# Kernel tuning notes

Measured on AMD Instinct MI355X. Metric: run time of the kernel, lower is better.

## Reference

```python
import jax, jax.numpy as jnp
import numpy as np

K_HEADS = 8
D_HEAD = 8
C_IN = 128   # c_x + c_t after channel concat
C_OUT = K_HEADS * D_HEAD  # 64
SMALL = -32767.0  # -2**15 + 1


def setup_inputs() -> dict:
    key = jax.random.key(0)
    ks = jax.random.split(key, 12)
    B, Cx, V, T = 8, 64, 200, 128
    x = jax.random.normal(ks[0], (B, Cx, V, T), dtype=jnp.float32)
    tem_embedding = jax.random.normal(ks[1], (B, Cx, V, T), dtype=jnp.float32)
    s = 0.05
    Wq = jax.random.normal(ks[2], (C_OUT, C_IN), dtype=jnp.float32) * s
    bq = jax.random.normal(ks[3], (C_OUT,), dtype=jnp.float32) * s
    Wk = jax.random.normal(ks[4], (C_OUT, C_IN), dtype=jnp.float32) * s
    bk = jax.random.normal(ks[5], (C_OUT,), dtype=jnp.float32) * s
    Wv = jax.random.normal(ks[6], (C_OUT, C_IN), dtype=jnp.float32) * s
    bv = jax.random.normal(ks[7], (C_OUT,), dtype=jnp.float32) * s
    Wo = jax.random.normal(ks[8], (C_OUT, C_OUT), dtype=jnp.float32) * s
    bo = jax.random.normal(ks[9], (C_OUT,), dtype=jnp.float32) * s
    return {"x": x, "tem_embedding": tem_embedding,
            "Wq": Wq, "bq": bq, "Wk": Wk, "bk": bk,
            "Wv": Wv, "bv": bv, "Wo": Wo, "bo": bo}


def reference(x, tem_embedding, Wq, bq, Wk, bk, Wv, bv, Wo, bo):
    B, _, V, T = x.shape
    # concat temporal embedding on channel dim (last T steps)
    xt = jnp.concatenate([x, tem_embedding[:, :, :, -T:]], axis=1)  # [B, C_IN, V, T]

    def proj(W, b):  # 1x1 conv == channel einsum
        return jnp.einsum('oi,bivt->bovt', W, xt) + b[None, :, None, None]

    def heads(t):  # [B, K*d, V, T] -> [K*B, V, T, d] (split on dim1, cat on dim0)
        t = t.reshape(B, K_HEADS, D_HEAD, V, T)
        t = jnp.transpose(t, (1, 0, 3, 4, 2))  # [K, B, V, T, d]
        return t.reshape(K_HEADS * B, V, T, D_HEAD)

    q = heads(proj(Wq, bq))
    k = heads(proj(Wk, bk))
    v = heads(proj(Wv, bv))

    attn = jnp.einsum('nvtd,nvsd->nvts', q, k) / jnp.sqrt(jnp.float32(D_HEAD))
    causal = jnp.tril(jnp.ones((T, T), dtype=bool))  # [T, T]
    attn = jnp.where(causal[None, None, :, :], attn, SMALL)
    attn = jax.nn.softmax(attn, axis=-1)
    out = jnp.einsum('nvts,nvsd->nvtd', attn, v)  # [K*B, V, T, d]

    # merge heads back: [K*B, V, T, d] -> [B, K*d, V, T]
    out = out.reshape(K_HEADS, B, V, T, D_HEAD)
    out = jnp.transpose(out, (1, 0, 4, 2, 3)).reshape(B, K_HEADS * D_HEAD, V, T)
    out = jnp.einsum('oi,bivt->bovt', Wo, out) + bo[None, :, None, None]
    return jax.nn.relu(out)
```

## Files before the change

### kernel.cpp

```cpp
#include <hip/hip_runtime.h>
#include <stdint.h>

#define TPB 512

constexpr int Bb   = 8;
constexpr int Vv   = 200;
constexpr int Tt   = 128;
constexpr int CIN  = 128;
constexpr int COUT = 64;

typedef __attribute__((ext_vector_type(8))) short bf16x8;
typedef __attribute__((ext_vector_type(4))) short short4v;
typedef __attribute__((ext_vector_type(4))) float f32x4;

__device__ __forceinline__ unsigned short f2bf(float f) {
    union { float f; unsigned u; } x; x.f = f;
    unsigned r = x.u + 0x7fffu + ((x.u >> 16) & 1u);
    return (unsigned short)(r >> 16);
}
__device__ __forceinline__ unsigned pk2(float a, float b) {
    return (unsigned)f2bf(a) | ((unsigned)f2bf(b) << 16);
}

#if __has_builtin(__builtin_amdgcn_mfma_f32_16x16x16bf16_1k)
#define MFMA16(a, b, c) __builtin_amdgcn_mfma_f32_16x16x16bf16_1k(a, b, c, 0, 0, 0)
#else
__device__ __forceinline__ f32x4 mfma16_asm(short4v a, short4v b, f32x4 c) {
    f32x4 d;
    asm("v_mfma_f32_16x16x16_bf16 %0, %1, %2, %3" : "=v"(d) : "v"(a), "v"(b), "v"(c));
    return d;
}
#define MFMA16(a, b, c) mfma16_asm(a, b, c)
#endif

__global__ __launch_bounds__(TPB, 6)
void tatt_fused(const float* __restrict__ x, const float* __restrict__ tem,
                const float* __restrict__ Wq, const float* __restrict__ bq,
                const float* __restrict__ Wk, const float* __restrict__ bk,
                const float* __restrict__ Wv, const float* __restrict__ bv,
                const float* __restrict__ Wo, const float* __restrict__ bo,
                float* __restrict__ out)
{
    __shared__ __align__(16) unsigned char smem[53248];
    unsigned short* qk = (unsigned short*)smem;
    unsigned short* vt = (unsigned short*)(smem + 32768);
    unsigned short* ot = (unsigned short*)(smem + 32768);
    unsigned short* xt = (unsigned short*)(smem + 49152);

    const int tid = threadIdx.x;
    const int w = tid >> 6, lane = tid & 63;
    const int l15 = lane & 15, qd = lane >> 4;
    const int b = blockIdx.x / Vv, v = blockIdx.x % Vv;
    const float QS = 1.44269504088896f * 0.35355339059327f;

    bf16x8 afr0[4], afr1[4];
    {
        const float* W0 = (w < 4) ? Wq : Wv;
        const int o0_ = (w < 4) ? w : (w - 4);
        const float* base0 = W0 + (o0_ * 16 + l15) * CIN + qd * 8;
        #pragma unroll
        for (int kc = 0; kc < 4; ++kc) {
            float4 fa = *(const float4*)(base0 + kc * 32);
            float4 fb = *(const float4*)(base0 + kc * 32 + 4);
            union { bf16x8 v8; unsigned u[4]; } t;
            t.u[0] = pk2(fa.x, fa.y); t.u[1] = pk2(fa.z, fa.w);
            t.u[2] = pk2(fb.x, fb.y); t.u[3] = pk2(fb.z, fb.w);
            afr0[kc] = t.v8;
        }
        if (w < 4) {
            const float* base1 = Wk + (w * 16 + l15) * CIN + qd * 8;
            #pragma unroll
            for (int kc = 0; kc < 4; ++kc) {
                float4 fa = *(const float4*)(base1 + kc * 32);
                float4 fb = *(const float4*)(base1 + kc * 32 + 4);
                union { bf16x8 v8; unsigned u[4]; } t;
                t.u[0] = pk2(fa.x, fa.y); t.u[1] = pk2(fa.z, fa.w);
                t.u[2] = pk2(fb.x, fb.y); t.u[3] = pk2(fb.z, fb.w);
                afr1[kc] = t.v8;
            }
        }
    }

    auto tileC = [&](const bf16x8 (&A)[4], int p, int ot_, int r) {
        f32x4 acc = {0.f, 0.f, 0.f, 0.f};
        const unsigned short* Bbp = xt + l15 * CIN;
        #pragma unroll
        for (int kc = 0; kc < 4; ++kc) {
            int phys = (kc * 4 + qd) ^ l15;
            bf16x8 bb = *(const bf16x8*)(Bbp + phys * 8);
            acc = __builtin_amdgcn_mfma_f32_16x16x32_bf16(A[kc], bb, acc, 0, 0, 0);
        }
        const int obase = ot_ * 16 + qd * 4;
        const float* bp = (p == 0) ? bq : ((p == 1) ? bk : bv);
        float4 bias = *(const float4*)(bp + obase);
        float bb4[4] = {bias.x, bias.y, bias.z, bias.w};
        const int tg = r * 16 + l15;
        if (p == 2) {
            #pragma unroll
            for (int rr = 0; rr < 4; ++rr) {
                int dg = obase + rr;
                int tp = tg ^ ((((dg >> 2) & 3)) << 4);
                vt[dg * 128 + tp] = f2bf(acc[rr] + bb4[rr]);
            }
        } else {
            float sc = (p == 0) ? QS : 1.0f;
            ushort4 s4;
            s4.x = f2bf((acc[0] + bb4[0]) * sc);
            s4.y = f2bf((acc[1] + bb4[1]) * sc);
            s4.z = f2bf((acc[2] + bb4[2]) * sc);
            s4.w = f2bf((acc[3] + bb4[3]) * sc);
            int phys = (obase >> 2) ^ (tg & 14);
            *(ushort4*)(qk + p * 8192 + tg * 64 + phys * 4) = s4;
        }
    };

    {
        const int sc_ = tid >> 2;
        const int stq = tid & 3;
        const float* sbase = (sc_ < 64 ? x : tem)
            + ((b * 64 + (sc_ & 63)) * Vv + v) * Tt + stq * 4;
        float4 pf = *(const float4*)(sbase);
        const int clow = sc_ & 7, chi = sc_ >> 3;

        for (int r = 0; r < 8; ++r) {
            if (r) __syncthreads();
            {
                int t0 = stq * 4;
                xt[(t0 + 0) * CIN + ((chi ^ (t0 + 0)) << 3) + clow] = f2bf(pf.x);
                xt[(t0 + 1) * CIN + ((chi ^ (t0 + 1)) << 3) + clow] = f2bf(pf.y);
                xt[(t0 + 2) * CIN + ((chi ^ (t0 + 2)) << 3) + clow] = f2bf(pf.z);
                xt[(t0 + 3) * CIN + ((chi ^ (t0 + 3)) << 3) + clow] = f2bf(pf.w);
            }
            if (r < 7) pf = *(const float4*)(sbase + (r + 1) * 16);
            __syncthreads();
            if (w < 4) { tileC(afr0, 0, w, r); tileC(afr1, 1, w, r); }
            else       { tileC(afr0, 2, w - 4, r); }
        }
    }
    __syncthreads();

    {
        const int h = w;
        const int qkoff = ((h * 2 + qd) ^ (l15 & 14)) << 2;
        short4v vfrag[8];
        short4v qfrag[8];
        {
            const int dg = h * 8 + l15;
            const int swz = ((dg >> 2) & 3) << 4;
            #pragma unroll
            for (int st = 0; st < 8; ++st) {
                short4v f = {0, 0, 0, 0};
                if (l15 < 8) {
                    int sp = (st * 16 + qd * 4) ^ swz;
                    f = *(const short4v*)(vt + dg * 128 + sp);
                }
                vfrag[st] = f;
            }
            #pragma unroll
            for (int st = 0; st < 8; ++st) {
                short4v qf = {0, 0, 0, 0};
                if (qd < 2) qf = *(const short4v*)(qk + (st * 16 + l15) * 64 + qkoff);
                qfrag[st] = qf;
            }
        }
        __syncthreads();

        bool dmask[4];
        #pragma unroll
        for (int r = 0; r < 4; ++r) dmask[r] = (qd * 4 + r) <= l15;

        #pragma unroll
        for (int tt = 0; tt < 8; ++tt) {
            f32x4 o0 = {0.f, 0.f, 0.f, 0.f}, o1 = {0.f, 0.f, 0.f, 0.f};
            float lac = 0.f;
            #pragma unroll
            for (int st = 0; st < 8; ++st) {
                if (st <= tt) {
                    short4v kf = {0, 0, 0, 0};
                    if (qd < 2) kf = *(const short4v*)(qk + 8192 + (st * 16 + l15) * 64 + qkoff);
                    f32x4 z = {0.f, 0.f, 0.f, 0.f};
                    f32x4 s = MFMA16(kf, qfrag[tt], z);
                    float p0 = __builtin_amdgcn_exp2f(s[0]);
                    float p1 = __builtin_amdgcn_exp2f(s[1]);
                    float p2 = __builtin_amdgcn_exp2f(s[2]);
                    float p3 = __builtin_amdgcn_exp2f(s[3]);
                    if (st == tt) {
                        p0 = dmask[0] ? p0 : 0.f;
                        p1 = dmask[1] ? p1 : 0.f;
                        p2 = dmask[2] ? p2 : 0.f;
                        p3 = dmask[3] ? p3 : 0.f;
                    }
                    lac += (p0 + p1) + (p2 + p3);
                    int pp0 = (int)pk2(p0, p1), pp1 = (int)pk2(p2, p3);
                    short4v pf;
                    pf[0] = (short)(pp0 & 0xffff); pf[1] = (short)(pp0 >> 16);
                    pf[2] = (short)(pp1 & 0xffff); pf[3] = (short)(pp1 >> 16);
                    if (st & 1) o1 = MFMA16(vfrag[st], pf, o1);
                    else        o0 = MFMA16(vfrag[st], pf, o0);
                }
            }
            float l = lac;
            l += __shfl_xor(l, 16, 64);
            l += __shfl_xor(l, 32, 64);
            float rl = __builtin_amdgcn_rcpf(l);
            if (qd < 2) {
                float r0 = (o0[0] + o1[0]) * rl, r1 = (o0[1] + o1[1]) * rl;
                float r2 = (o0[2] + o1[2]) * rl, r3 = (o0[3] + o1[3]) * rl;
                int t = tt * 16 + l15;
                uint2 st2;
                st2.x = pk2(r0, r1);
                st2.y = pk2(r2, r3);
                *(uint2*)(ot + t * 64 + (((h * 2 + qd) ^ (l15 & 14)) << 2)) = st2;
            }
        }
    }
    __syncthreads();

    {
        const int tq3 = w & 3, ohB = (w >> 2) * 2;
        bf16x8 wof[2][2];
        #pragma unroll
        for (int oth = 0; oth < 2; ++oth) {
            const float* base = Wo + ((ohB + oth) * 16 + l15) * COUT + qd * 8;
            #pragma unroll
            for (int kc = 0; kc < 2; ++kc) {
                float4 fa = *(const float4*)(base + kc * 32);
                float4 fb = *(const float4*)(base + kc * 32 + 4);
                union { bf16x8 v8; unsigned u[4]; } t;
                t.u[0] = pk2(fa.x, fa.y); t.u[1] = pk2(fa.z, fa.w);
                t.u[2] = pk2(fb.x, fb.y); t.u[3] = pk2(fb.z, fb.w);
                wof[oth][kc] = t.v8;
            }
        }
        const int tt0 = tq3 * 2, tt1 = tq3 * 2 + 1;
        f32x4 aA0 = {0.f, 0.f, 0.f, 0.f}, aA1 = {0.f, 0.f, 0.f, 0.f};
        f32x4 aB0 = {0.f, 0.f, 0.f, 0.f}, aB1 = {0.f, 0.f, 0.f, 0.f};
        #pragma unroll
        for (int kc = 0; kc < 2; ++kc) {
            const int off = ((kc * 8 + qd * 2) ^ (l15 & 14)) << 2;
            bf16x8 b0 = *(const bf16x8*)(ot + (tt0 * 16 + l15) * 64 + off);
            bf16x8 b1 = *(const bf16x8*)(ot + (tt1 * 16 + l15) * 64 + off);
            aA0 = __builtin_amdgcn_mfma_f32_16x16x32_bf16(wof[0][kc], b0, aA0, 0, 0, 0);
            aA1 = __builtin_amdgcn_mfma_f32_16x16x32_bf16(wof[1][kc], b0, aA1, 0, 0, 0);
            aB0 = __builtin_amdgcn_mfma_f32_16x16x32_bf16(wof[0][kc], b1, aB0, 0, 0, 0);
            aB1 = __builtin_amdgcn_mfma_f32_16x16x32_bf16(wof[1][kc], b1, aB1, 0, 0, 0);
        }
        #pragma unroll
        for (int oth = 0; oth < 2; ++oth) {
            const int obase = (ohB + oth) * 16 + qd * 4;
            float4 bias = *(const float4*)(bo + obase);
            float bb4[4] = {bias.x, bias.y, bias.z, bias.w};
            const f32x4& c0 = oth ? aA1 : aA0;
            const f32x4& c1 = oth ? aB1 : aB0;
            #pragma unroll
            for (int rr = 0; rr < 4; ++rr) {
                float v0 = c0[rr] + bb4[rr]; v0 = v0 > 0.f ? v0 : 0.f;
                float v1 = c1[rr] + bb4[rr]; v1 = v1 > 0.f ? v1 : 0.f;
                float* po = out + ((b * COUT + obase + rr) * Vv + v) * Tt
                            + tq3 * 32 + l15;
                po[0]  = v0;
                po[16] = v1;
            }
        }
    }
}

extern "C" void kernel_launch(void* const* d_in, const int* in_sizes, int n_in,
                              void* d_out, int out_size, void* d_ws, size_t ws_size,
                              hipStream_t stream) {
    (void)in_sizes; (void)n_in; (void)ws_size; (void)out_size; (void)d_ws;
    const float* x   = (const float*)d_in[0];
    const float* tem = (const float*)d_in[1];
    const float* Wq  = (const float*)d_in[2];
    const float* bq  = (const float*)d_in[3];
    const float* Wk  = (const float*)d_in[4];
    const float* bk  = (const float*)d_in[5];
    const float* Wv  = (const float*)d_in[6];
    const float* bv  = (const float*)d_in[7];
    const float* Wo  = (const float*)d_in[8];
    const float* bo  = (const float*)d_in[9];
    float* out = (float*)d_out;

    tatt_fused<<<dim3(Bb * Vv), dim3(TPB), 0, stream>>>(
        x, tem, Wq, bq, Wk, bk, Wv, bv, Wo, bo, out);
}
```

Before: 224.0 us.

## Stream Q tiles through a small LDS buffer into registers to cut LDS footprint

Q is no longer stored as a full 128x64 tile in LDS. Each 16-row Q tile is written to a 2 KB scratch buffer and pulled into register fragments on the next projection iteration, with the last tile read after the loop. This shrinks shared memory from about 52 KB to 38 KB per block, so more blocks can fit per CU, and the launch bound is raised to match. The cost is that Q fragments stay live in registers through the projection loop, and the tighter register cap that comes with higher occupancy could cause spills.

```diff
diff --git a/kernel.cpp b/kernel.cpp
--- a/kernel.cpp
+++ b/kernel.cpp
@@ -33,7 +33,7 @@
 #define MFMA16(a, b, c) mfma16_asm(a, b, c)
 #endif
 
-__global__ __launch_bounds__(TPB, 6)
+__global__ __launch_bounds__(TPB, 8)
 void tatt_fused(const float* __restrict__ x, const float* __restrict__ tem,
                 const float* __restrict__ Wq, const float* __restrict__ bq,
                 const float* __restrict__ Wk, const float* __restrict__ bk,
@@ -41,17 +41,20 @@
                 const float* __restrict__ Wo, const float* __restrict__ bo,
                 float* __restrict__ out)
 {
-    __shared__ __align__(16) unsigned char smem[53248];
-    unsigned short* qk = (unsigned short*)smem;
-    unsigned short* vt = (unsigned short*)(smem + 32768);
-    unsigned short* ot = (unsigned short*)(smem + 32768);
-    unsigned short* xt = (unsigned short*)(smem + 49152);
+    __shared__ __align__(16) unsigned char smem[38912];
+    unsigned short* kbuf = (unsigned short*)smem;
+    unsigned short* vt   = (unsigned short*)(smem + 16384);
+    unsigned short* ot   = (unsigned short*)(smem + 16384);
+    unsigned short* xt   = (unsigned short*)(smem + 32768);
+    unsigned short* qbuf = (unsigned short*)(smem + 36864);
 
     const int tid = threadIdx.x;
     const int w = tid >> 6, lane = tid & 63;
     const int l15 = lane & 15, qd = lane >> 4;
     const int b = blockIdx.x / Vv, v = blockIdx.x % Vv;
     const float QS = 1.44269504088896f * 0.35355339059327f;
+
+    const int qkoff = ((w * 2 + qd) ^ (l15 & 14)) << 2;
 
     bf16x8 afr0[4], afr1[4];
     {
@@ -102,17 +105,26 @@
                 int tp = tg ^ ((((dg >> 2) & 3)) << 4);
                 vt[dg * 128 + tp] = f2bf(acc[rr] + bb4[rr]);
             }
+        } else if (p == 1) {
+            ushort4 s4;
+            s4.x = f2bf(acc[0] + bb4[0]);
+            s4.y = f2bf(acc[1] + bb4[1]);
+            s4.z = f2bf(acc[2] + bb4[2]);
+            s4.w = f2bf(acc[3] + bb4[3]);
+            int phys = (obase >> 2) ^ (tg & 14);
+            *(ushort4*)(kbuf + tg * 64 + phys * 4) = s4;
         } else {
-            float sc = (p == 0) ? QS : 1.0f;
             ushort4 s4;
-            s4.x = f2bf((acc[0] + bb4[0]) * sc);
-            s4.y = f2bf((acc[1] + bb4[1]) * sc);
-            s4.z = f2bf((acc[2] + bb4[2]) * sc);
-            s4.w = f2bf((acc[3] + bb4[3]) * sc);
-            int phys = (obase >> 2) ^ (tg & 14);
-            *(ushort4*)(qk + p * 8192 + tg * 64 + phys * 4) = s4;
+            s4.x = f2bf((acc[0] + bb4[0]) * QS);
+            s4.y = f2bf((acc[1] + bb4[1]) * QS);
+            s4.z = f2bf((acc[2] + bb4[2]) * QS);
+            s4.w = f2bf((acc[3] + bb4[3]) * QS);
+            int phys = (obase >> 2) ^ (l15 & 14);
+            *(ushort4*)(qbuf + l15 * 64 + phys * 4) = s4;
         }
     };
+
+    short4v qfrag[8];
 
     {
         const int sc_ = tid >> 2;
@@ -122,8 +134,15 @@
         float4 pf = *(const float4*)(sbase);
         const int clow = sc_ & 7, chi = sc_ >> 3;
 
+        #pragma unroll
         for (int r = 0; r < 8; ++r) {
             if (r) __syncthreads();
+            if (r) {
+                short4v qf = {0, 0, 0, 0};
+                if (qd < 2)
+                    qf = *(const short4v*)(qbuf + l15 * 64 + qkoff);
+                qfrag[r - 1] = qf;
+            }
             {
                 int t0 = stq * 4;
                 xt[(t0 + 0) * CIN + ((chi ^ (t0 + 0)) << 3) + clow] = f2bf(pf.x);
@@ -141,9 +160,12 @@
 
     {
         const int h = w;
-        const int qkoff = ((h * 2 + qd) ^ (l15 & 14)) << 2;
+        {
+            short4v qf = {0, 0, 0, 0};
+            if (qd < 2) qf = *(const short4v*)(qbuf + l15 * 64 + qkoff);
+            qfrag[7] = qf;
+        }
         short4v vfrag[8];
-        short4v qfrag[8];
         {
             const int dg = h * 8 + l15;
             const int swz = ((dg >> 2) & 3) << 4;
@@ -156,12 +178,6 @@
                 }
                 vfrag[st] = f;
             }
-            #pragma unroll
-            for (int st = 0; st < 8; ++st) {
-                short4v qf = {0, 0, 0, 0};
-                if (qd < 2) qf = *(const short4v*)(qk + (st * 16 + l15) * 64 + qkoff);
-                qfrag[st] = qf;
-            }
         }
         __syncthreads();
 
@@ -177,7 +193,7 @@
             for (int st = 0; st < 8; ++st) {
                 if (st <= tt) {
                     short4v kf = {0, 0, 0, 0};
-                    if (qd < 2) kf = *(const short4v*)(qk + 8192 + (st * 16 + l15) * 64 + qkoff);
+                    if (qd < 2) kf = *(const short4v*)(kbuf + (st * 16 + l15) * 64 + qkoff);
                     f32x4 z = {0.f, 0.f, 0.f, 0.f};
                     f32x4 s = MFMA16(kf, qfrag[tt], z);
                     float p0 = __builtin_amdgcn_exp2f(s[0]);
```

After: 279.5 us. 24.7% more time.
